# Kernel optimization log

Hardware: AMD Instinct MI355X
Metric: run time of the kernel (lower is better)

## Reference

```python
import jax, jax.numpy as jnp
import numpy as np
from jax import lax

KERNEL = 15
IGNORE = 255


def setup_inputs() -> dict:
    key = jax.random.key(0)
    k1, k2 = jax.random.split(key)
    B, C, H, W = 32, 2, 480, 864
    logits = jax.random.normal(k1, (B, C, H, W), dtype=jnp.float32)
    labels = jax.random.randint(k2, (B, H, W), 0, 2, dtype=jnp.int32)
    return {"logits": logits, "labels": labels}


def _boundary_edgemap(labels):
    # labels: [B, H, W] int32 with values in {0, 1, IGNORE}
    lbl = labels.astype(jnp.int32)
    # np_label = label*255, with ignore pixels set to 0 (matches cv2 path)
    np_label = jnp.where(lbl == IGNORE, 0, lbl * 255)
    win = (1, KERNEL, KERNEL)
    strides = (1, 1, 1)
    # cv2.erode with ones kernel == 15x15 min filter (border value +inf -> pad 255)
    erosion = lax.reduce_window(np_label, jnp.int32(255), lax.min, win, strides, "SAME")
    # cv2.dilate == 15x15 max filter (border value -inf -> pad 0)
    dilation = lax.reduce_window(np_label, jnp.int32(0), lax.max, win, strides, "SAME")
    boundary = dilation - erosion  # >0 exactly on the morphological boundary band
    edgemap = jnp.where(boundary > 0, lbl, IGNORE)
    edgemap = jnp.where(lbl == IGNORE, IGNORE, edgemap)
    return edgemap


def reference(logits, labels):
    # logits: [B, C, H, W] log-probabilities, labels: [B, H, W]
    edgemap = _boundary_edgemap(labels)  # [B, H, W]
    valid = edgemap != IGNORE
    tgt = jnp.where(valid, edgemap, 0)  # safe index for ignored pixels
    # gather logits[b, tgt, h, w] -> [B, H, W]
    picked = jnp.take_along_axis(logits, tgt[:, None, :, :], axis=1)[:, 0]
    # NLLLoss with ignore_index: mean of -logp over valid pixels
    n_valid = jnp.maximum(jnp.sum(valid), 1)
    loss = -jnp.sum(jnp.where(valid, picked, 0.0)) / n_valid.astype(logits.dtype)
    return loss
```

## Files before the change

kernel.cpp:

```cpp
#include <hip/hip_runtime.h>


namespace {
constexpr int B_ = 32;
constexpr int H_ = 480;
constexpr int W_ = 864;
constexpr int HW = H_ * W_;
constexpr int R_ = 7;
constexpr int TH_ = 8;
constexpr int LH = TH_ + 2 * R_;
constexpr int SW = 216;
constexpr int NSX = W_ / SW;
constexpr int NSY = H_ / TH_;
constexpr int WPB = 4;
constexpr int NTILE = B_ * NSY * NSX;
constexpr int NBLKP = NTILE / WPB;
}

__device__ __forceinline__ unsigned long long shfl_up64(unsigned long long x, int d) {
  return __shfl_up(x, d, 64);
}
__device__ __forceinline__ unsigned long long shfl_dn64(unsigned long long x, int d) {
  return __shfl_down(x, d, 64);
}

extern "C" __global__ __launch_bounds__(256, 2)
void boundary_loss_main(const float* __restrict__ logits,
                        const int* __restrict__ labels,
                        double2* __restrict__ partials)
{
  __shared__ double red_s[WPB];
  __shared__ unsigned red_c[WPB];

  const int tid = threadIdx.x;
  const int lane = tid & 63;
  const int wv = tid >> 6;
  const int t = blockIdx.x * WPB + wv;
  const int b = t / (NSY * NSX);
  const int rr = t - b * (NSY * NSX);
  const int sy = rr >> 2;
  const int sx = rr & 3;

  const int gr0 = sy * TH_;
  const int wb = sx * SW - 8;
  const int cb0 = wb + 4 * lane;
  const bool colinb = (cb0 >= 0) && (cb0 + 3 < W_);
  const int cbc = colinb ? cb0 : (cb0 < 0 ? 0 : W_ - 4);

  const int* __restrict__ lab = labels + b * HW + cbc;
  const float* __restrict__ lg = logits + (size_t)(2 * b) * HW;

  unsigned long long f0 = 0, f1 = 0, f2 = 0, f3 = 0;
  unsigned cp0 = 0, cp1 = 0, cp2 = 0, cp3 = 0;
#pragma unroll
  for (int a = 0; a < LH; ++a) {
    int gr = gr0 - R_ + a;
    gr = gr < 0 ? 0 : (gr >= H_ ? H_ - 1 : gr);
    const int4 v = *(const int4*)(lab + gr * W_);
    const unsigned e1x = (v.x == 1), e1y = (v.y == 1),
                   e1z = (v.z == 1), e1w = (v.w == 1);
    f0 |= (unsigned long long)(1u + e1x) << (2 * a);
    f1 |= (unsigned long long)(1u + e1y) << (2 * a);
    f2 |= (unsigned long long)(1u + e1z) << (2 * a);
    f3 |= (unsigned long long)(1u + e1w) << (2 * a);
    if (a >= R_ && a < R_ + TH_) {
      const int sh = 2 * (a - R_);
      cp0 |= (e1x | ((unsigned)(v.x == 255) << 1)) << sh;
      cp1 |= (e1y | ((unsigned)(v.y == 255) << 1)) << sh;
      cp2 |= (e1z | ((unsigned)(v.z == 255) << 1)) << sh;
      cp3 |= (e1w | ((unsigned)(v.w == 255) << 1)) << sh;
    }
  }
  {
    const int tv = gr0 == 0 ? R_ : 0;
    const int hi = LH < (487 - gr0) ? LH : (487 - gr0);
    unsigned long long rm = ((1ull << (2 * (hi - tv))) - 1ull) << (2 * tv);
    if (!colinb) rm = 0;
    f0 &= rm; f1 &= rm; f2 &= rm; f3 &= rm;
  }

  const bool outl = (lane >= 2) && (lane < 56);
  float4 g0[TH_], g1[TH_];
  if (outl) {
    const float* pg = lg + (size_t)gr0 * W_ + cb0;
#pragma unroll
    for (int o = 0; o < TH_; ++o) {
      g0[o] = *(const float4*)(pg + o * W_);
      g1[o] = *(const float4*)(pg + o * W_ + HW);
    }
  }

  const unsigned long long allf = f0 | f1 | f2 | f3;
  const unsigned long long s2 = f2 | f3, s3 = f1 | s2;
  const unsigned long long p2 = f0 | f1, p3 = p2 | f2;
  const unsigned long long core =
      shfl_up64(allf, 1) | allf | shfl_dn64(allf, 1);
  unsigned long long w0 = core | shfl_up64(s3, 2);
  unsigned long long w1 = core | shfl_up64(s2, 2) | shfl_dn64(f0, 2);
  unsigned long long w2 = core | shfl_up64(f3, 2) | shfl_dn64(p2, 2);
  unsigned long long w3 = core | shfl_dn64(p3, 2);

  w0 |= w0 >> 2;  w0 |= w0 >> 4;  w0 |= w0 >> 8;  w0 |= w0 >> 14;
  w1 |= w1 >> 2;  w1 |= w1 >> 4;  w1 |= w1 >> 8;  w1 |= w1 >> 14;
  w2 |= w2 >> 2;  w2 |= w2 >> 4;  w2 |= w2 >> 8;  w2 |= w2 >> 14;
  w3 |= w3 >> 2;  w3 |= w3 >> 4;  w3 |= w3 >> 8;  w3 |= w3 >> 14;

  double lsum = 0.0;
  unsigned lcnt = 0;
  if (outl) {
#pragma unroll
    for (int o = 0; o < TH_; ++o) {
      const unsigned b0 = (unsigned)(w0 >> (2 * o)) & 3u;
      const unsigned b1 = (unsigned)(w1 >> (2 * o)) & 3u;
      const unsigned b2 = (unsigned)(w2 >> (2 * o)) & 3u;
      const unsigned b3 = (unsigned)(w3 >> (2 * o)) & 3u;
      const unsigned q0 = (cp0 >> (2 * o)) & 3u;
      const unsigned q1 = (cp1 >> (2 * o)) & 3u;
      const unsigned q2 = (cp2 >> (2 * o)) & 3u;
      const unsigned q3 = (cp3 >> (2 * o)) & 3u;
      const float4 a = g0[o], c = g1[o];
      const bool k0 = (b0 == 3u) && !(q0 & 2u);
      const bool k1 = (b1 == 3u) && !(q1 & 2u);
      const bool k2 = (b2 == 3u) && !(q2 & 2u);
      const bool k3 = (b3 == 3u) && !(q3 & 2u);
      lsum += k0 ? (double)((q0 & 1u) ? c.x : a.x) : 0.0;
      lsum += k1 ? (double)((q1 & 1u) ? c.y : a.y) : 0.0;
      lsum += k2 ? (double)((q2 & 1u) ? c.z : a.z) : 0.0;
      lsum += k3 ? (double)((q3 & 1u) ? c.w : a.w) : 0.0;
      lcnt += (unsigned)k0 + k1 + k2 + k3;
    }
  }

#pragma unroll
  for (int off = 32; off > 0; off >>= 1) {
    lsum += __shfl_down(lsum, off, 64);
    lcnt += __shfl_down(lcnt, off, 64);
  }
  if ((tid & 63) == 0) { red_s[wv] = lsum; red_c[wv] = lcnt; }
  __syncthreads();
  if (tid == 0) {
    const double s = red_s[0] + red_s[1] + red_s[2] + red_s[3];
    const double c = (double)(red_c[0] + red_c[1] + red_c[2] + red_c[3]);
    partials[blockIdx.x] = make_double2(s, c);
  }
}

extern "C" __global__ __launch_bounds__(1024)
void boundary_loss_final(const double2* __restrict__ partials,
                         float* __restrict__ out)
{
  __shared__ double red_s[16];
  __shared__ double red_c[16];
  const int tid = threadIdx.x;
  double s = 0.0, c = 0.0;
  for (int i = tid; i < NBLKP; i += 1024) {
    const double2 p = partials[i];
    s += p.x;
    c += p.y;
  }
#pragma unroll
  for (int off = 32; off > 0; off >>= 1) {
    s += __shfl_down(s, off, 64);
    c += __shfl_down(c, off, 64);
  }
  const int wave = tid >> 6;
  if ((tid & 63) == 0) { red_s[wave] = s; red_c[wave] = c; }
  __syncthreads();
  if (tid == 0) {
    double ts = 0.0, tc = 0.0;
#pragma unroll
    for (int i = 0; i < 16; ++i) { ts += red_s[i]; tc += red_c[i]; }
    if (tc < 1.0) tc = 1.0;
    out[0] = (float)(-ts / tc);
  }
}

extern "C" void kernel_launch(void* const* d_in, const int* in_sizes, int n_in,
                              void* d_out, int out_size, void* d_ws, size_t ws_size,
                              hipStream_t stream)
{
  const float* logits = (const float*)d_in[0];
  const int* labels = (const int*)d_in[1];
  float* out = (float*)d_out;
  double2* partials = (double2*)d_ws;

  boundary_loss_main<<<dim3(NBLKP), 256, 0, stream>>>(logits, labels, partials);
  boundary_loss_final<<<1, 1024, 0, stream>>>(partials, out);
}
```

Baseline: 191.9 us.

## Use taller 32-row tiles with single-wave blocks and double-buffered logit loads

Tile height grows from 8 to 32 rows, so the 14-row label halo is a smaller share of each tile and fewer labels are read again. The column bitmasks now span two 64-bit words, and a carried vertical fold handles them. Blocks become one wave each, with a remapped block index, and the LDS reduction is removed. Logit loads are issued in 8-row groups with a ping-pong buffer so loads overlap the boundary computation. The cost is more registers per lane and fewer waves overall, which may reduce the latency hiding the old layout got from having many waves in flight.

```diff
diff --git a/kernel.cpp b/kernel.cpp
--- a/kernel.cpp
+++ b/kernel.cpp
@@ -7,142 +7,166 @@
 constexpr int W_ = 864;
 constexpr int HW = H_ * W_;
 constexpr int R_ = 7;
-constexpr int TH_ = 8;
+constexpr int TH_ = 32;
 constexpr int LH = TH_ + 2 * R_;
 constexpr int SW = 216;
 constexpr int NSX = W_ / SW;
 constexpr int NSY = H_ / TH_;
-constexpr int WPB = 4;
 constexpr int NTILE = B_ * NSY * NSX;
-constexpr int NBLKP = NTILE / WPB;
-}
-
-__device__ __forceinline__ unsigned long long shfl_up64(unsigned long long x, int d) {
+}
+
+typedef unsigned long long u64;
+
+__device__ __forceinline__ u64 shfl_up64(u64 x, int d) {
   return __shfl_up(x, d, 64);
 }
-__device__ __forceinline__ unsigned long long shfl_dn64(unsigned long long x, int d) {
+__device__ __forceinline__ u64 shfl_dn64(u64 x, int d) {
   return __shfl_down(x, d, 64);
 }
 
-extern "C" __global__ __launch_bounds__(256, 2)
+__device__ __forceinline__ void vfold15(u64& lo, u64 hi) {
+  u64 l = lo, h = hi;
+  l |= (l >> 2) | (h << 62);   h |= h >> 2;
+  l |= (l >> 4) | (h << 60);   h |= h >> 4;
+  l |= (l >> 8) | (h << 56);   h |= h >> 8;
+  l |= (l >> 14) | (h << 50);
+  lo = l;
+}
+
+extern "C" __global__ __launch_bounds__(64, 2)
 void boundary_loss_main(const float* __restrict__ logits,
                         const int* __restrict__ labels,
                         double2* __restrict__ partials)
 {
-  __shared__ double red_s[WPB];
-  __shared__ unsigned red_c[WPB];
-
-  const int tid = threadIdx.x;
-  const int lane = tid & 63;
-  const int wv = tid >> 6;
-  const int t = blockIdx.x * WPB + wv;
-  const int b = t / (NSY * NSX);
-  const int rr = t - b * (NSY * NSX);
+  const int lane = threadIdx.x;
+  const int bid = blockIdx.x;
+  const int lb = (bid & 7) * (NTILE / 8) + (bid >> 3);
+  const int b = lb / (NSY * NSX);
+  const int rr = lb - b * (NSY * NSX);
   const int sy = rr >> 2;
   const int sx = rr & 3;
 
   const int gr0 = sy * TH_;
-  const int wb = sx * SW - 8;
-  const int cb0 = wb + 4 * lane;
+  const int cb0 = sx * SW - 8 + 4 * lane;
   const bool colinb = (cb0 >= 0) && (cb0 + 3 < W_);
   const int cbc = colinb ? cb0 : (cb0 < 0 ? 0 : W_ - 4);
 
   const int* __restrict__ lab = labels + b * HW + cbc;
   const float* __restrict__ lg = logits + (size_t)(2 * b) * HW;
 
-  unsigned long long f0 = 0, f1 = 0, f2 = 0, f3 = 0;
-  unsigned cp0 = 0, cp1 = 0, cp2 = 0, cp3 = 0;
+  u64 fL0 = 0, fL1 = 0, fL2 = 0, fL3 = 0;
+  u64 fH0 = 0, fH1 = 0, fH2 = 0, fH3 = 0;
+  u64 cp0 = 0, cp1 = 0, cp2 = 0, cp3 = 0;
 #pragma unroll
   for (int a = 0; a < LH; ++a) {
     int gr = gr0 - R_ + a;
     gr = gr < 0 ? 0 : (gr >= H_ ? H_ - 1 : gr);
     const int4 v = *(const int4*)(lab + gr * W_);
-    const unsigned e1x = (v.x == 1), e1y = (v.y == 1),
-                   e1z = (v.z == 1), e1w = (v.w == 1);
-    f0 |= (unsigned long long)(1u + e1x) << (2 * a);
-    f1 |= (unsigned long long)(1u + e1y) << (2 * a);
-    f2 |= (unsigned long long)(1u + e1z) << (2 * a);
-    f3 |= (unsigned long long)(1u + e1w) << (2 * a);
+    const u64 e1x = (v.x == 1), e1y = (v.y == 1),
+              e1z = (v.z == 1), e1w = (v.w == 1);
+    if (a < 32) {
+      const int sh = 2 * a;
+      fL0 |= (1ull + e1x) << sh;  fL1 |= (1ull + e1y) << sh;
+      fL2 |= (1ull + e1z) << sh;  fL3 |= (1ull + e1w) << sh;
+    } else {
+      const int sh = 2 * (a - 32);
+      fH0 |= (1ull + e1x) << sh;  fH1 |= (1ull + e1y) << sh;
+      fH2 |= (1ull + e1z) << sh;  fH3 |= (1ull + e1w) << sh;
+    }
     if (a >= R_ && a < R_ + TH_) {
       const int sh = 2 * (a - R_);
-      cp0 |= (e1x | ((unsigned)(v.x == 255) << 1)) << sh;
-      cp1 |= (e1y | ((unsigned)(v.y == 255) << 1)) << sh;
-      cp2 |= (e1z | ((unsigned)(v.z == 255) << 1)) << sh;
-      cp3 |= (e1w | ((unsigned)(v.w == 255) << 1)) << sh;
+      cp0 |= (e1x | ((u64)(v.x == 255) << 1)) << sh;
+      cp1 |= (e1y | ((u64)(v.y == 255) << 1)) << sh;
+      cp2 |= (e1z | ((u64)(v.z == 255) << 1)) << sh;
+      cp3 |= (e1w | ((u64)(v.w == 255) << 1)) << sh;
     }
   }
   {
-    const int tv = gr0 == 0 ? R_ : 0;
-    const int hi = LH < (487 - gr0) ? LH : (487 - gr0);
-    unsigned long long rm = ((1ull << (2 * (hi - tv))) - 1ull) << (2 * tv);
-    if (!colinb) rm = 0;
-    f0 &= rm; f1 &= rm; f2 &= rm; f3 &= rm;
+    u64 mLo = ~0ull, mHi = (1ull << 28) - 1;
+    if (gr0 == 0) mLo &= (~0ull) << (2 * R_);
+    if (gr0 == H_ - TH_) mHi &= (1ull << 14) - 1;
+    if (!colinb) { mLo = 0; mHi = 0; }
+    fL0 &= mLo; fL1 &= mLo; fL2 &= mLo; fL3 &= mLo;
+    fH0 &= mHi; fH1 &= mHi; fH2 &= mHi; fH3 &= mHi;
   }
 
   const bool outl = (lane >= 2) && (lane < 56);
-  float4 g0[TH_], g1[TH_];
-  if (outl) {
-    const float* pg = lg + (size_t)gr0 * W_ + cb0;
-#pragma unroll
-    for (int o = 0; o < TH_; ++o) {
-      g0[o] = *(const float4*)(pg + o * W_);
-      g1[o] = *(const float4*)(pg + o * W_ + HW);
-    }
-  }
-
-  const unsigned long long allf = f0 | f1 | f2 | f3;
-  const unsigned long long s2 = f2 | f3, s3 = f1 | s2;
-  const unsigned long long p2 = f0 | f1, p3 = p2 | f2;
-  const unsigned long long core =
-      shfl_up64(allf, 1) | allf | shfl_dn64(allf, 1);
-  unsigned long long w0 = core | shfl_up64(s3, 2);
-  unsigned long long w1 = core | shfl_up64(s2, 2) | shfl_dn64(f0, 2);
-  unsigned long long w2 = core | shfl_up64(f3, 2) | shfl_dn64(p2, 2);
-  unsigned long long w3 = core | shfl_dn64(p3, 2);
-
-  w0 |= w0 >> 2;  w0 |= w0 >> 4;  w0 |= w0 >> 8;  w0 |= w0 >> 14;
-  w1 |= w1 >> 2;  w1 |= w1 >> 4;  w1 |= w1 >> 8;  w1 |= w1 >> 14;
-  w2 |= w2 >> 2;  w2 |= w2 >> 4;  w2 |= w2 >> 8;  w2 |= w2 >> 14;
-  w3 |= w3 >> 2;  w3 |= w3 >> 4;  w3 |= w3 >> 8;  w3 |= w3 >> 14;
+  const float* pg = lg + (size_t)gr0 * W_ + cbc;
+  float4 ga0[8], ga1[8];
+  float4 gb0[8], gb1[8];
+#define ISSUE(G0, G1, grp)                                                  \
+  if (outl) {                                                               \
+    const float* p_ = pg + (size_t)(8 * (grp)) * W_;                        \
+    _Pragma("unroll") for (int o = 0; o < 8; ++o) {                         \
+      G0[o] = *(const float4*)(p_ + (size_t)o * W_);                        \
+      G1[o] = *(const float4*)(p_ + (size_t)o * W_ + HW);                   \
+    }                                                                       \
+  }
+  ISSUE(ga0, ga1, 0)
+
+  const u64 allL = fL0 | fL1 | fL2 | fL3, allH = fH0 | fH1 | fH2 | fH3;
+  const u64 s2L = fL2 | fL3, s2H = fH2 | fH3;
+  const u64 s3L = fL1 | s2L, s3H = fH1 | s2H;
+  const u64 p2L = fL0 | fL1, p2H = fH0 | fH1;
+  const u64 p3L = p2L | fL2, p3H = p2H | fH2;
+  const u64 coreL = shfl_up64(allL, 1) | allL | shfl_dn64(allL, 1);
+  const u64 coreH = shfl_up64(allH, 1) | allH | shfl_dn64(allH, 1);
+  u64 w0L = coreL | shfl_up64(s3L, 2);
+  u64 w0H = coreH | shfl_up64(s3H, 2);
+  u64 w1L = coreL | shfl_up64(s2L, 2) | shfl_dn64(fL0, 2);
+  u64 w1H = coreH | shfl_up64(s2H, 2) | shfl_dn64(fH0, 2);
+  u64 w2L = coreL | shfl_up64(fL3, 2) | shfl_dn64(p2L, 2);
+  u64 w2H = coreH | shfl_up64(fH3, 2) | shfl_dn64(p2H, 2);
+  u64 w3L = coreL | shfl_dn64(p3L, 2);
+  u64 w3H = coreH | shfl_dn64(p3H, 2);
+
+  vfold15(w0L, w0H);
+  vfold15(w1L, w1H);
+  vfold15(w2L, w2H);
+  vfold15(w3L, w3H);
 
   double lsum = 0.0;
   unsigned lcnt = 0;
-  if (outl) {
-#pragma unroll
-    for (int o = 0; o < TH_; ++o) {
-      const unsigned b0 = (unsigned)(w0 >> (2 * o)) & 3u;
-      const unsigned b1 = (unsigned)(w1 >> (2 * o)) & 3u;
-      const unsigned b2 = (unsigned)(w2 >> (2 * o)) & 3u;
-      const unsigned b3 = (unsigned)(w3 >> (2 * o)) & 3u;
-      const unsigned q0 = (cp0 >> (2 * o)) & 3u;
-      const unsigned q1 = (cp1 >> (2 * o)) & 3u;
-      const unsigned q2 = (cp2 >> (2 * o)) & 3u;
-      const unsigned q3 = (cp3 >> (2 * o)) & 3u;
-      const float4 a = g0[o], c = g1[o];
-      const bool k0 = (b0 == 3u) && !(q0 & 2u);
-      const bool k1 = (b1 == 3u) && !(q1 & 2u);
-      const bool k2 = (b2 == 3u) && !(q2 & 2u);
-      const bool k3 = (b3 == 3u) && !(q3 & 2u);
-      lsum += k0 ? (double)((q0 & 1u) ? c.x : a.x) : 0.0;
-      lsum += k1 ? (double)((q1 & 1u) ? c.y : a.y) : 0.0;
-      lsum += k2 ? (double)((q2 & 1u) ? c.z : a.z) : 0.0;
-      lsum += k3 ? (double)((q3 & 1u) ? c.w : a.w) : 0.0;
-      lcnt += (unsigned)k0 + k1 + k2 + k3;
-    }
-  }
+#define CONSUME(G0, G1, grp)                                                \
+  if (outl) {                                                               \
+    _Pragma("unroll") for (int o = 0; o < 8; ++o) {                         \
+      const int ro = 8 * (grp) + o;                                         \
+      const unsigned b0 = (unsigned)(w0L >> (2 * ro)) & 3u;                 \
+      const unsigned b1 = (unsigned)(w1L >> (2 * ro)) & 3u;                 \
+      const unsigned b2 = (unsigned)(w2L >> (2 * ro)) & 3u;                 \
+      const unsigned b3 = (unsigned)(w3L >> (2 * ro)) & 3u;                 \
+      const unsigned q0 = (unsigned)(cp0 >> (2 * ro)) & 3u;                 \
+      const unsigned q1 = (unsigned)(cp1 >> (2 * ro)) & 3u;                 \
+      const unsigned q2 = (unsigned)(cp2 >> (2 * ro)) & 3u;                 \
+      const unsigned q3 = (unsigned)(cp3 >> (2 * ro)) & 3u;                 \
+      const float4 A = G0[o], C = G1[o];                                    \
+      const bool k0 = (b0 == 3u) && !(q0 & 2u);                             \
+      const bool k1 = (b1 == 3u) && !(q1 & 2u);                             \
+      const bool k2 = (b2 == 3u) && !(q2 & 2u);                             \
+      const bool k3 = (b3 == 3u) && !(q3 & 2u);                             \
+      lsum += k0 ? (double)((q0 & 1u) ? C.x : A.x) : 0.0;                   \
+      lsum += k1 ? (double)((q1 & 1u) ? C.y : A.y) : 0.0;                   \
+      lsum += k2 ? (double)((q2 & 1u) ? C.z : A.z) : 0.0;                   \
+      lsum += k3 ? (double)((q3 & 1u) ? C.w : A.w) : 0.0;                   \
+      lcnt += (unsigned)k0 + k1 + k2 + k3;                                  \
+    }                                                                       \
+  }
+  ISSUE(gb0, gb1, 1)
+  CONSUME(ga0, ga1, 0)
+  ISSUE(ga0, ga1, 2)
+  CONSUME(gb0, gb1, 1)
+  ISSUE(gb0, gb1, 3)
+  CONSUME(ga0, ga1, 2)
+  CONSUME(gb0, gb1, 3)
+#undef ISSUE
+#undef CONSUME
 
 #pragma unroll
   for (int off = 32; off > 0; off >>= 1) {
     lsum += __shfl_down(lsum, off, 64);
     lcnt += __shfl_down(lcnt, off, 64);
   }
-  if ((tid & 63) == 0) { red_s[wv] = lsum; red_c[wv] = lcnt; }
-  __syncthreads();
-  if (tid == 0) {
-    const double s = red_s[0] + red_s[1] + red_s[2] + red_s[3];
-    const double c = (double)(red_c[0] + red_c[1] + red_c[2] + red_c[3]);
-    partials[blockIdx.x] = make_double2(s, c);
-  }
+  if (lane == 0) partials[bid] = make_double2(lsum, (double)lcnt);
 }
 
 extern "C" __global__ __launch_bounds__(1024)
@@ -153,7 +177,7 @@
   __shared__ double red_c[16];
   const int tid = threadIdx.x;
   double s = 0.0, c = 0.0;
-  for (int i = tid; i < NBLKP; i += 1024) {
+  for (int i = tid; i < NTILE; i += 1024) {
     const double2 p = partials[i];
     s += p.x;
     c += p.y;
@@ -184,6 +208,6 @@
   float* out = (float*)d_out;
   double2* partials = (double2*)d_ws;
 
-  boundary_loss_main<<<dim3(NBLKP), 256, 0, stream>>>(logits, labels, partials);
+  boundary_loss_main<<<dim3(NTILE), 64, 0, stream>>>(logits, labels, partials);
   boundary_loss_final<<<1, 1024, 0, stream>>>(partials, out);
 }
```

Result: slower. 197.7 us (+3.0%).

## Stream each wave over three row tiles, reusing horizontal-window label halo

Applied to the files above, without the earlier changes.

Each wave now handles a 24-row segment as three consecutive 8-row tiles. The horizontally windowed label bits and class codes for the 14-row vertical halo are carried from one tile to the next, so every tile loads only 8 new label rows instead of 22. The horizontal window is computed per loaded row, before the vertical OR-reduction, using 32-bit masks. The block-to-work mapping is swizzled across image chunks and launch bounds now target 4 blocks per CU. The cost is fewer blocks and waves in flight, plus a serial dependence between tiles inside each wave.

```diff
diff --git a/kernel.cpp b/kernel.cpp
--- a/kernel.cpp
+++ b/kernel.cpp
@@ -8,23 +8,31 @@
 constexpr int HW = H_ * W_;
 constexpr int R_ = 7;
 constexpr int TH_ = 8;
-constexpr int LH = TH_ + 2 * R_;
+constexpr int SEG = 3;
+constexpr int ORW = TH_ * SEG;
 constexpr int SW = 216;
 constexpr int NSX = W_ / SW;
-constexpr int NSY = H_ / TH_;
+constexpr int NSEG = H_ / ORW;
 constexpr int WPB = 4;
-constexpr int NTILE = B_ * NSY * NSX;
-constexpr int NBLKP = NTILE / WPB;
-}
-
-__device__ __forceinline__ unsigned long long shfl_up64(unsigned long long x, int d) {
-  return __shfl_up(x, d, 64);
-}
-__device__ __forceinline__ unsigned long long shfl_dn64(unsigned long long x, int d) {
-  return __shfl_down(x, d, 64);
-}
-
-extern "C" __global__ __launch_bounds__(256, 2)
+constexpr int NBLK = B_ * NSX * (NSEG / WPB);
+}
+
+typedef unsigned long long u64;
+
+__device__ __forceinline__ void hwin15_4(unsigned f0, unsigned f1, unsigned f2,
+                                         unsigned f3, unsigned& w0, unsigned& w1,
+                                         unsigned& w2, unsigned& w3) {
+  const unsigned allf = f0 | f1 | f2 | f3;
+  const unsigned s2 = f2 | f3, s3 = f1 | s2;
+  const unsigned p2 = f0 | f1, p3 = p2 | f2;
+  const unsigned core = __shfl_up(allf, 1, 64) | allf | __shfl_down(allf, 1, 64);
+  w0 = core | __shfl_up(s3, 2, 64);
+  w1 = core | __shfl_up(s2, 2, 64) | __shfl_down(f0, 2, 64);
+  w2 = core | __shfl_up(f3, 2, 64) | __shfl_down(p2, 2, 64);
+  w3 = core | __shfl_down(p3, 2, 64);
+}
+
+extern "C" __global__ __launch_bounds__(256, 4)
 void boundary_loss_main(const float* __restrict__ logits,
                         const int* __restrict__ labels,
                         double2* __restrict__ partials)
@@ -35,100 +43,129 @@
   const int tid = threadIdx.x;
   const int lane = tid & 63;
   const int wv = tid >> 6;
-  const int t = blockIdx.x * WPB + wv;
-  const int b = t / (NSY * NSX);
-  const int rr = t - b * (NSY * NSX);
-  const int sy = rr >> 2;
-  const int sx = rr & 3;
-
-  const int gr0 = sy * TH_;
-  const int wb = sx * SW - 8;
-  const int cb0 = wb + 4 * lane;
+  const int lb = (blockIdx.x & 7) * (NBLK / 8) + (blockIdx.x >> 3);
+  const int img = lb / 20;
+  const int r = lb - img * 20;
+  const int strip = r / 5;
+  const int segblk = r - strip * 5;
+  const int seg = segblk * WPB + wv;
+  const int gr0 = seg * ORW;
+
+  const int cb0 = strip * SW - 8 + 4 * lane;
   const bool colinb = (cb0 >= 0) && (cb0 + 3 < W_);
   const int cbc = colinb ? cb0 : (cb0 < 0 ? 0 : W_ - 4);
-
-  const int* __restrict__ lab = labels + b * HW + cbc;
-  const float* __restrict__ lg = logits + (size_t)(2 * b) * HW;
-
-  unsigned long long f0 = 0, f1 = 0, f2 = 0, f3 = 0;
-  unsigned cp0 = 0, cp1 = 0, cp2 = 0, cp3 = 0;
-#pragma unroll
-  for (int a = 0; a < LH; ++a) {
-    int gr = gr0 - R_ + a;
-    gr = gr < 0 ? 0 : (gr >= H_ ? H_ - 1 : gr);
-    const int4 v = *(const int4*)(lab + gr * W_);
-    const unsigned e1x = (v.x == 1), e1y = (v.y == 1),
-                   e1z = (v.z == 1), e1w = (v.w == 1);
-    f0 |= (unsigned long long)(1u + e1x) << (2 * a);
-    f1 |= (unsigned long long)(1u + e1y) << (2 * a);
-    f2 |= (unsigned long long)(1u + e1z) << (2 * a);
-    f3 |= (unsigned long long)(1u + e1w) << (2 * a);
-    if (a >= R_ && a < R_ + TH_) {
-      const int sh = 2 * (a - R_);
-      cp0 |= (e1x | ((unsigned)(v.x == 255) << 1)) << sh;
-      cp1 |= (e1y | ((unsigned)(v.y == 255) << 1)) << sh;
-      cp2 |= (e1z | ((unsigned)(v.z == 255) << 1)) << sh;
-      cp3 |= (e1w | ((unsigned)(v.w == 255) << 1)) << sh;
-    }
-  }
-  {
-    const int tv = gr0 == 0 ? R_ : 0;
-    const int hi = LH < (487 - gr0) ? LH : (487 - gr0);
-    unsigned long long rm = ((1ull << (2 * (hi - tv))) - 1ull) << (2 * tv);
-    if (!colinb) rm = 0;
-    f0 &= rm; f1 &= rm; f2 &= rm; f3 &= rm;
-  }
-
+  const bool labok = colinb && (lane < 58);
   const bool outl = (lane >= 2) && (lane < 56);
-  float4 g0[TH_], g1[TH_];
-  if (outl) {
-    const float* pg = lg + (size_t)gr0 * W_ + cb0;
-#pragma unroll
-    for (int o = 0; o < TH_; ++o) {
-      g0[o] = *(const float4*)(pg + o * W_);
-      g1[o] = *(const float4*)(pg + o * W_ + HW);
-    }
-  }
-
-  const unsigned long long allf = f0 | f1 | f2 | f3;
-  const unsigned long long s2 = f2 | f3, s3 = f1 | s2;
-  const unsigned long long p2 = f0 | f1, p3 = p2 | f2;
-  const unsigned long long core =
-      shfl_up64(allf, 1) | allf | shfl_dn64(allf, 1);
-  unsigned long long w0 = core | shfl_up64(s3, 2);
-  unsigned long long w1 = core | shfl_up64(s2, 2) | shfl_dn64(f0, 2);
-  unsigned long long w2 = core | shfl_up64(f3, 2) | shfl_dn64(p2, 2);
-  unsigned long long w3 = core | shfl_dn64(p3, 2);
-
-  w0 |= w0 >> 2;  w0 |= w0 >> 4;  w0 |= w0 >> 8;  w0 |= w0 >> 14;
-  w1 |= w1 >> 2;  w1 |= w1 >> 4;  w1 |= w1 >> 8;  w1 |= w1 >> 14;
-  w2 |= w2 >> 2;  w2 |= w2 >> 4;  w2 |= w2 >> 8;  w2 |= w2 >> 14;
-  w3 |= w3 >> 2;  w3 |= w3 >> 4;  w3 |= w3 >> 8;  w3 |= w3 >> 14;
+
+  const int* __restrict__ lab = labels + img * HW + cbc;
+  const float* __restrict__ lg = logits + (size_t)(2 * img) * HW;
+  const float* pg = lg + (size_t)gr0 * W_ + cb0;
+
+  unsigned pf0 = 0, pf1 = 0, pf2 = 0, pf3 = 0;
+  u64 Cst0 = 0, Cst1 = 0, Cst2 = 0, Cst3 = 0;
+#pragma unroll
+  for (int a = 0; a < 14; ++a) {
+    const int gr = gr0 - R_ + a;
+    const int grc = gr < 0 ? 0 : gr;
+    const int4 v = *(const int4*)(lab + grc * W_);
+    const unsigned m = (labok && gr >= 0) ? 3u : 0u;
+    const int sh = 2 * a;
+    pf0 |= (((v.x == 1) ? 2u : 1u) & m) << sh;
+    pf1 |= (((v.y == 1) ? 2u : 1u) & m) << sh;
+    pf2 |= (((v.z == 1) ? 2u : 1u) & m) << sh;
+    pf3 |= (((v.w == 1) ? 2u : 1u) & m) << sh;
+    Cst0 |= (u64)(((v.x == 1) ? 1u : 0u) | ((v.x == 255) ? 2u : 0u)) << sh;
+    Cst1 |= (u64)(((v.y == 1) ? 1u : 0u) | ((v.y == 255) ? 2u : 0u)) << sh;
+    Cst2 |= (u64)(((v.z == 1) ? 1u : 0u) | ((v.z == 255) ? 2u : 0u)) << sh;
+    Cst3 |= (u64)(((v.w == 1) ? 1u : 0u) | ((v.w == 255) ? 2u : 0u)) << sh;
+  }
+  unsigned Wst0, Wst1, Wst2, Wst3;
+  hwin15_4(pf0, pf1, pf2, pf3, Wst0, Wst1, Wst2, Wst3);
 
   double lsum = 0.0;
   unsigned lcnt = 0;
-  if (outl) {
-#pragma unroll
-    for (int o = 0; o < TH_; ++o) {
-      const unsigned b0 = (unsigned)(w0 >> (2 * o)) & 3u;
-      const unsigned b1 = (unsigned)(w1 >> (2 * o)) & 3u;
-      const unsigned b2 = (unsigned)(w2 >> (2 * o)) & 3u;
-      const unsigned b3 = (unsigned)(w3 >> (2 * o)) & 3u;
-      const unsigned q0 = (cp0 >> (2 * o)) & 3u;
-      const unsigned q1 = (cp1 >> (2 * o)) & 3u;
-      const unsigned q2 = (cp2 >> (2 * o)) & 3u;
-      const unsigned q3 = (cp3 >> (2 * o)) & 3u;
-      const float4 a = g0[o], c = g1[o];
-      const bool k0 = (b0 == 3u) && !(q0 & 2u);
-      const bool k1 = (b1 == 3u) && !(q1 & 2u);
-      const bool k2 = (b2 == 3u) && !(q2 & 2u);
-      const bool k3 = (b3 == 3u) && !(q3 & 2u);
-      lsum += k0 ? (double)((q0 & 1u) ? c.x : a.x) : 0.0;
-      lsum += k1 ? (double)((q1 & 1u) ? c.y : a.y) : 0.0;
-      lsum += k2 ? (double)((q2 & 1u) ? c.z : a.z) : 0.0;
-      lsum += k3 ? (double)((q3 & 1u) ? c.w : a.w) : 0.0;
-      lcnt += (unsigned)k0 + k1 + k2 + k3;
+
+  for (int s = 0; s < SEG; ++s) {
+    const int y = gr0 + s * TH_;
+
+    float4 g0[TH_], g1[TH_];
+    if (outl) {
+      const float* p_ = pg + (size_t)(s * TH_) * W_;
+#pragma unroll
+      for (int o = 0; o < TH_; ++o) {
+        g0[o] = *(const float4*)(p_ + (size_t)o * W_);
+        g1[o] = *(const float4*)(p_ + (size_t)o * W_ + HW);
+      }
     }
+
+    unsigned nf0 = 0, nf1 = 0, nf2 = 0, nf3 = 0;
+    u64 nc0 = 0, nc1 = 0, nc2 = 0, nc3 = 0;
+#pragma unroll
+    for (int k = 0; k < TH_; ++k) {
+      const int gr = y + R_ + k;
+      const int grc = gr >= H_ ? H_ - 1 : gr;
+      const int4 v = *(const int4*)(lab + grc * W_);
+      const unsigned m = (labok && gr < H_) ? 3u : 0u;
+      const int sh = 2 * k;
+      nf0 |= (((v.x == 1) ? 2u : 1u) & m) << sh;
+      nf1 |= (((v.y == 1) ? 2u : 1u) & m) << sh;
+      nf2 |= (((v.z == 1) ? 2u : 1u) & m) << sh;
+      nf3 |= (((v.w == 1) ? 2u : 1u) & m) << sh;
+      nc0 |= (u64)(((v.x == 1) ? 1u : 0u) | ((v.x == 255) ? 2u : 0u)) << sh;
+      nc1 |= (u64)(((v.y == 1) ? 1u : 0u) | ((v.y == 255) ? 2u : 0u)) << sh;
+      nc2 |= (u64)(((v.z == 1) ? 1u : 0u) | ((v.z == 255) ? 2u : 0u)) << sh;
+      nc3 |= (u64)(((v.w == 1) ? 1u : 0u) | ((v.w == 255) ? 2u : 0u)) << sh;
+    }
+
+    unsigned nw0, nw1, nw2, nw3;
+    hwin15_4(nf0, nf1, nf2, nf3, nw0, nw1, nw2, nw3);
+    const u64 F0 = (u64)Wst0 | ((u64)nw0 << 28);
+    const u64 F1 = (u64)Wst1 | ((u64)nw1 << 28);
+    const u64 F2 = (u64)Wst2 | ((u64)nw2 << 28);
+    const u64 F3 = (u64)Wst3 | ((u64)nw3 << 28);
+    const u64 Cc0 = Cst0 | (nc0 << 28);
+    const u64 Cc1 = Cst1 | (nc1 << 28);
+    const u64 Cc2 = Cst2 | (nc2 << 28);
+    const u64 Cc3 = Cst3 | (nc3 << 28);
+
+    u64 V0 = F0, V1 = F1, V2 = F2, V3 = F3;
+    V0 |= V0 >> 2;  V0 |= V0 >> 4;  V0 |= V0 >> 8;  V0 |= V0 >> 14;
+    V1 |= V1 >> 2;  V1 |= V1 >> 4;  V1 |= V1 >> 8;  V1 |= V1 >> 14;
+    V2 |= V2 >> 2;  V2 |= V2 >> 4;  V2 |= V2 >> 8;  V2 |= V2 >> 14;
+    V3 |= V3 >> 2;  V3 |= V3 >> 4;  V3 |= V3 >> 8;  V3 |= V3 >> 14;
+
+    if (outl) {
+#pragma unroll
+      for (int o = 0; o < TH_; ++o) {
+        const unsigned b0 = (unsigned)(V0 >> (2 * o)) & 3u;
+        const unsigned b1 = (unsigned)(V1 >> (2 * o)) & 3u;
+        const unsigned b2 = (unsigned)(V2 >> (2 * o)) & 3u;
+        const unsigned b3 = (unsigned)(V3 >> (2 * o)) & 3u;
+        const unsigned q0 = (unsigned)(Cc0 >> (14 + 2 * o)) & 3u;
+        const unsigned q1 = (unsigned)(Cc1 >> (14 + 2 * o)) & 3u;
+        const unsigned q2 = (unsigned)(Cc2 >> (14 + 2 * o)) & 3u;
+        const unsigned q3 = (unsigned)(Cc3 >> (14 + 2 * o)) & 3u;
+        const float4 a = g0[o], c = g1[o];
+        const bool k0 = (b0 == 3u) && !(q0 & 2u);
+        const bool k1 = (b1 == 3u) && !(q1 & 2u);
+        const bool k2 = (b2 == 3u) && !(q2 & 2u);
+        const bool k3 = (b3 == 3u) && !(q3 & 2u);
+        lsum += k0 ? (double)((q0 & 1u) ? c.x : a.x) : 0.0;
+        lsum += k1 ? (double)((q1 & 1u) ? c.y : a.y) : 0.0;
+        lsum += k2 ? (double)((q2 & 1u) ? c.z : a.z) : 0.0;
+        lsum += k3 ? (double)((q3 & 1u) ? c.w : a.w) : 0.0;
+        lcnt += (unsigned)k0 + k1 + k2 + k3;
+      }
+    }
+
+    Wst0 = (unsigned)(F0 >> 16) & 0x0FFFFFFFu;
+    Wst1 = (unsigned)(F1 >> 16) & 0x0FFFFFFFu;
+    Wst2 = (unsigned)(F2 >> 16) & 0x0FFFFFFFu;
+    Wst3 = (unsigned)(F3 >> 16) & 0x0FFFFFFFu;
+    Cst0 = (Cc0 >> 16) & 0x0FFFFFFFull;
+    Cst1 = (Cc1 >> 16) & 0x0FFFFFFFull;
+    Cst2 = (Cc2 >> 16) & 0x0FFFFFFFull;
+    Cst3 = (Cc3 >> 16) & 0x0FFFFFFFull;
   }
 
 #pragma unroll
@@ -153,7 +190,7 @@
   __shared__ double red_c[16];
   const int tid = threadIdx.x;
   double s = 0.0, c = 0.0;
-  for (int i = tid; i < NBLKP; i += 1024) {
+  for (int i = tid; i < NBLK; i += 1024) {
     const double2 p = partials[i];
     s += p.x;
     c += p.y;
@@ -184,6 +221,6 @@
   float* out = (float*)d_out;
   double2* partials = (double2*)d_ws;
 
-  boundary_loss_main<<<dim3(NBLKP), 256, 0, stream>>>(logits, labels, partials);
+  boundary_loss_main<<<dim3(NBLK), 256, 0, stream>>>(logits, labels, partials);
   boundary_loss_final<<<1, 1024, 0, stream>>>(partials, out);
 }
```

Result: slower. 201.9 us (+5.2%).

## Use taller 16-row tiles with single-wave blocks and XCD-aware block mapping

Applied to the files above, without the earlier changes.

Doubles the rows each wave produces from 8 to 16. The label halo overhead per output row then drops from 22/8 to 30/16 rows read. Blocks become single 64-thread waves that write partials directly, which removes the shared-memory reduction and the block barrier. Block IDs are remapped in groups of eight, likely to spread work across XCDs, and the strip/segment order is changed for locality. The logits loads are split into two 8-row batches to limit register pressure, at the cost of less memory-level parallelism per wave and more partials.

```diff
diff --git a/kernel.cpp b/kernel.cpp
--- a/kernel.cpp
+++ b/kernel.cpp
@@ -7,50 +7,48 @@
 constexpr int W_ = 864;
 constexpr int HW = H_ * W_;
 constexpr int R_ = 7;
-constexpr int TH_ = 8;
+constexpr int TH_ = 16;
 constexpr int LH = TH_ + 2 * R_;
 constexpr int SW = 216;
 constexpr int NSX = W_ / SW;
 constexpr int NSY = H_ / TH_;
-constexpr int WPB = 4;
-constexpr int NTILE = B_ * NSY * NSX;
-constexpr int NBLKP = NTILE / WPB;
-}
-
-__device__ __forceinline__ unsigned long long shfl_up64(unsigned long long x, int d) {
+constexpr int NBLK = B_ * NSX * NSY;
+}
+
+typedef unsigned long long u64;
+
+__device__ __forceinline__ u64 shfl_up64(u64 x, int d) {
   return __shfl_up(x, d, 64);
 }
-__device__ __forceinline__ unsigned long long shfl_dn64(unsigned long long x, int d) {
+__device__ __forceinline__ u64 shfl_dn64(u64 x, int d) {
   return __shfl_down(x, d, 64);
 }
 
-extern "C" __global__ __launch_bounds__(256, 2)
+extern "C" __global__ __launch_bounds__(64, 4)
 void boundary_loss_main(const float* __restrict__ logits,
                         const int* __restrict__ labels,
                         double2* __restrict__ partials)
 {
-  __shared__ double red_s[WPB];
-  __shared__ unsigned red_c[WPB];
-
-  const int tid = threadIdx.x;
-  const int lane = tid & 63;
-  const int wv = tid >> 6;
-  const int t = blockIdx.x * WPB + wv;
-  const int b = t / (NSY * NSX);
-  const int rr = t - b * (NSY * NSX);
-  const int sy = rr >> 2;
-  const int sx = rr & 3;
-
-  const int gr0 = sy * TH_;
-  const int wb = sx * SW - 8;
-  const int cb0 = wb + 4 * lane;
+  const int lane = threadIdx.x;
+  const int bid = blockIdx.x;
+  const int lb = (bid & 7) * (NBLK / 8) + (bid >> 3);
+  const int img = lb / (NSX * NSY);
+  const int r = lb - img * (NSX * NSY);
+  const int strip = r / NSY;
+  const int seg = r - strip * NSY;
+  const int gr0 = seg * TH_;
+
+  const int cb0 = strip * SW - 8 + 4 * lane;
   const bool colinb = (cb0 >= 0) && (cb0 + 3 < W_);
   const int cbc = colinb ? cb0 : (cb0 < 0 ? 0 : W_ - 4);
-
-  const int* __restrict__ lab = labels + b * HW + cbc;
-  const float* __restrict__ lg = logits + (size_t)(2 * b) * HW;
-
-  unsigned long long f0 = 0, f1 = 0, f2 = 0, f3 = 0;
+  const bool labok = colinb && (lane < 58);
+  const bool outl = (lane >= 2) && (lane < 56);
+
+  const int* __restrict__ lab = labels + img * HW + cbc;
+  const float* __restrict__ lg = logits + (size_t)(2 * img) * HW;
+  const float* pg = lg + (size_t)gr0 * W_ + cb0;
+
+  u64 f0 = 0, f1 = 0, f2 = 0, f3 = 0;
   unsigned cp0 = 0, cp1 = 0, cp2 = 0, cp3 = 0;
 #pragma unroll
   for (int a = 0; a < LH; ++a) {
@@ -59,10 +57,10 @@
     const int4 v = *(const int4*)(lab + gr * W_);
     const unsigned e1x = (v.x == 1), e1y = (v.y == 1),
                    e1z = (v.z == 1), e1w = (v.w == 1);
-    f0 |= (unsigned long long)(1u + e1x) << (2 * a);
-    f1 |= (unsigned long long)(1u + e1y) << (2 * a);
-    f2 |= (unsigned long long)(1u + e1z) << (2 * a);
-    f3 |= (unsigned long long)(1u + e1w) << (2 * a);
+    f0 |= (u64)(1u + e1x) << (2 * a);
+    f1 |= (u64)(1u + e1y) << (2 * a);
+    f2 |= (u64)(1u + e1z) << (2 * a);
+    f3 |= (u64)(1u + e1w) << (2 * a);
     if (a >= R_ && a < R_ + TH_) {
       const int sh = 2 * (a - R_);
       cp0 |= (e1x | ((unsigned)(v.x == 255) << 1)) << sh;
@@ -73,32 +71,32 @@
   }
   {
     const int tv = gr0 == 0 ? R_ : 0;
-    const int hi = LH < (487 - gr0) ? LH : (487 - gr0);
-    unsigned long long rm = ((1ull << (2 * (hi - tv))) - 1ull) << (2 * tv);
+    const int hi = LH < (H_ + R_ - gr0) ? LH : (H_ + R_ - gr0);
+    u64 rm = (hi - tv >= 32) ? ((((1ull << (2 * (hi - tv) - 32)) - 1ull) << 32)
+                                | 0xFFFFFFFFull)
+                             : ((1ull << (2 * (hi - tv))) - 1ull);
+    rm <<= 2 * tv;
     if (!colinb) rm = 0;
     f0 &= rm; f1 &= rm; f2 &= rm; f3 &= rm;
   }
 
-  const bool outl = (lane >= 2) && (lane < 56);
-  float4 g0[TH_], g1[TH_];
+  float4 a0[8], a1[8];
   if (outl) {
-    const float* pg = lg + (size_t)gr0 * W_ + cb0;
-#pragma unroll
-    for (int o = 0; o < TH_; ++o) {
-      g0[o] = *(const float4*)(pg + o * W_);
-      g1[o] = *(const float4*)(pg + o * W_ + HW);
-    }
-  }
-
-  const unsigned long long allf = f0 | f1 | f2 | f3;
-  const unsigned long long s2 = f2 | f3, s3 = f1 | s2;
-  const unsigned long long p2 = f0 | f1, p3 = p2 | f2;
-  const unsigned long long core =
-      shfl_up64(allf, 1) | allf | shfl_dn64(allf, 1);
-  unsigned long long w0 = core | shfl_up64(s3, 2);
-  unsigned long long w1 = core | shfl_up64(s2, 2) | shfl_dn64(f0, 2);
-  unsigned long long w2 = core | shfl_up64(f3, 2) | shfl_dn64(p2, 2);
-  unsigned long long w3 = core | shfl_dn64(p3, 2);
+#pragma unroll
+    for (int o = 0; o < 8; ++o) {
+      a0[o] = *(const float4*)(pg + (size_t)o * W_);
+      a1[o] = *(const float4*)(pg + (size_t)o * W_ + HW);
+    }
+  }
+
+  const u64 allf = f0 | f1 | f2 | f3;
+  const u64 s2 = f2 | f3, s3 = f1 | s2;
+  const u64 p2 = f0 | f1, p3 = p2 | f2;
+  const u64 core = shfl_up64(allf, 1) | allf | shfl_dn64(allf, 1);
+  u64 w0 = core | shfl_up64(s3, 2);
+  u64 w1 = core | shfl_up64(s2, 2) | shfl_dn64(f0, 2);
+  u64 w2 = core | shfl_up64(f3, 2) | shfl_dn64(p2, 2);
+  u64 w3 = core | shfl_dn64(p3, 2);
 
   w0 |= w0 >> 2;  w0 |= w0 >> 4;  w0 |= w0 >> 8;  w0 |= w0 >> 14;
   w1 |= w1 >> 2;  w1 |= w1 >> 4;  w1 |= w1 >> 8;  w1 |= w1 >> 14;
@@ -107,9 +105,10 @@
 
   double lsum = 0.0;
   unsigned lcnt = 0;
+
   if (outl) {
 #pragma unroll
-    for (int o = 0; o < TH_; ++o) {
+    for (int o = 0; o < 8; ++o) {
       const unsigned b0 = (unsigned)(w0 >> (2 * o)) & 3u;
       const unsigned b1 = (unsigned)(w1 >> (2 * o)) & 3u;
       const unsigned b2 = (unsigned)(w2 >> (2 * o)) & 3u;
@@ -118,7 +117,7 @@
       const unsigned q1 = (cp1 >> (2 * o)) & 3u;
       const unsigned q2 = (cp2 >> (2 * o)) & 3u;
       const unsigned q3 = (cp3 >> (2 * o)) & 3u;
-      const float4 a = g0[o], c = g1[o];
+      const float4 a = a0[o], c = a1[o];
       const bool k0 = (b0 == 3u) && !(q0 & 2u);
       const bool k1 = (b1 == 3u) && !(q1 & 2u);
       const bool k2 = (b2 == 3u) && !(q2 & 2u);
@@ -130,19 +129,44 @@
       lcnt += (unsigned)k0 + k1 + k2 + k3;
     }
   }
+  float4 b0v[8], b1v[8];
+  if (outl) {
+    const float* p_ = pg + (size_t)8 * W_;
+#pragma unroll
+    for (int o = 0; o < 8; ++o) {
+      b0v[o] = *(const float4*)(p_ + (size_t)o * W_);
+      b1v[o] = *(const float4*)(p_ + (size_t)o * W_ + HW);
+    }
+#pragma unroll
+    for (int o = 0; o < 8; ++o) {
+      const int ro = 8 + o;
+      const unsigned b0 = (unsigned)(w0 >> (2 * ro)) & 3u;
+      const unsigned b1 = (unsigned)(w1 >> (2 * ro)) & 3u;
+      const unsigned b2 = (unsigned)(w2 >> (2 * ro)) & 3u;
+      const unsigned b3 = (unsigned)(w3 >> (2 * ro)) & 3u;
+      const unsigned q0 = (cp0 >> (2 * ro)) & 3u;
+      const unsigned q1 = (cp1 >> (2 * ro)) & 3u;
+      const unsigned q2 = (cp2 >> (2 * ro)) & 3u;
+      const unsigned q3 = (cp3 >> (2 * ro)) & 3u;
+      const float4 a = b0v[o], c = b1v[o];
+      const bool k0 = (b0 == 3u) && !(q0 & 2u);
+      const bool k1 = (b1 == 3u) && !(q1 & 2u);
+      const bool k2 = (b2 == 3u) && !(q2 & 2u);
+      const bool k3 = (b3 == 3u) && !(q3 & 2u);
+      lsum += k0 ? (double)((q0 & 1u) ? c.x : a.x) : 0.0;
+      lsum += k1 ? (double)((q1 & 1u) ? c.y : a.y) : 0.0;
+      lsum += k2 ? (double)((q2 & 1u) ? c.z : a.z) : 0.0;
+      lsum += k3 ? (double)((q3 & 1u) ? c.w : a.w) : 0.0;
+      lcnt += (unsigned)k0 + k1 + k2 + k3;
+    }
+  }
 
 #pragma unroll
   for (int off = 32; off > 0; off >>= 1) {
     lsum += __shfl_down(lsum, off, 64);
     lcnt += __shfl_down(lcnt, off, 64);
   }
-  if ((tid & 63) == 0) { red_s[wv] = lsum; red_c[wv] = lcnt; }
-  __syncthreads();
-  if (tid == 0) {
-    const double s = red_s[0] + red_s[1] + red_s[2] + red_s[3];
-    const double c = (double)(red_c[0] + red_c[1] + red_c[2] + red_c[3]);
-    partials[blockIdx.x] = make_double2(s, c);
-  }
+  if (lane == 0) partials[bid] = make_double2(lsum, (double)lcnt);
 }
 
 extern "C" __global__ __launch_bounds__(1024)
@@ -153,7 +177,7 @@
   __shared__ double red_c[16];
   const int tid = threadIdx.x;
   double s = 0.0, c = 0.0;
-  for (int i = tid; i < NBLKP; i += 1024) {
+  for (int i = tid; i < NBLK; i += 1024) {
     const double2 p = partials[i];
     s += p.x;
     c += p.y;
@@ -184,6 +208,6 @@
   float* out = (float*)d_out;
   double2* partials = (double2*)d_ws;
 
-  boundary_loss_main<<<dim3(NBLKP), 256, 0, stream>>>(logits, labels, partials);
+  boundary_loss_main<<<dim3(NBLK), 64, 0, stream>>>(logits, labels, partials);
   boundary_loss_final<<<1, 1024, 0, stream>>>(partials, out);
 }
```

After: 219.5 us. 1.14x slower.
